# Kernel optimization log

Measured on AMD Instinct MI355X. Metric: run time of the kernel, lower is better.

## Reference

```python
import jax, jax.numpy as jnp
import numpy as np

B, D_IN, D, H, HD, M = 4096, 512, 128, 8, 16, 128
L = M + 1            # 1 query token + M memory slots
D_FF = 512
SCALE = 0.25         # 1/sqrt(HD)


def _ln(x, w, b, eps=1e-5):
    m = jnp.mean(x, axis=-1, keepdims=True)
    v = jnp.var(x, axis=-1, keepdims=True)
    return (x - m) * jax.lax.rsqrt(v + eps) * w + b


def setup_inputs() -> dict:
    ks = jax.random.split(jax.random.key(0), 26)
    n = lambda i, shape, s=1.0: jax.random.normal(ks[i], shape, jnp.float32) * s
    return {
        "x": n(0, (B, 1, D_IN)),
        "W_in": n(1, (D, D_IN), 0.05),
        "b_in": n(2, (D,), 0.02),
        "pos": n(3, (B, 1, D), 0.02),
        "mask": jnp.zeros((B, M), jnp.float32),  # additive attention bias for memory slots
        "mem": n(5, (B, M, D)),
        "ln1_w": jnp.ones((D,), jnp.float32), "ln1_b": jnp.zeros((D,), jnp.float32),
        "W_qkv": n(8, (3 * D, D), 0.09),
        "b_qkv": n(9, (3 * D,), 0.02),
        "W_out": n(10, (D, D), 0.09),
        "b_out": n(11, (D,), 0.02),
        "ln2_w": jnp.ones((D,), jnp.float32), "ln2_b": jnp.zeros((D,), jnp.float32),
        "ln3_w": jnp.ones((D,), jnp.float32), "ln3_b": jnp.zeros((D,), jnp.float32),
        "W_ff1": n(16, (D_FF, D), 0.09),
        "b_ff1": n(17, (D_FF,), 0.02),
        "ln4_w": jnp.ones((D_FF,), jnp.float32), "ln4_b": jnp.zeros((D_FF,), jnp.float32),
        "W_ff2": n(20, (D, D_FF), 0.04),
        "b_ff2": n(21, (D,), 0.02),
        "ln5_w": jnp.ones((D,), jnp.float32), "ln5_b": jnp.zeros((D,), jnp.float32),
        "W_head": n(24, (D_IN, D), 0.09),
        "b_head": n(25, (D_IN,), 0.02),
    }


def reference(x, W_in, b_in, pos, mask, mem, ln1_w, ln1_b, W_qkv, b_qkv,
              W_out, b_out, ln2_w, ln2_b, ln3_w, ln3_b, W_ff1, b_ff1,
              ln4_w, ln4_b, W_ff2, b_ff2, ln5_w, ln5_b, W_head, b_head):
    Bn = x.shape[0]
    # input projection + positional offset -> single query token per row  [B,1,D]
    q_in = (x.reshape(Bn, D_IN) @ W_in.T + b_in)[:, None, :] + pos
    # additive attention bias: 0 for the query slot, `mask` for memory slots  [B,L]
    bias = jnp.concatenate([jnp.zeros((Bn, 1), x.dtype), mask], axis=1)
    kv_in = jnp.concatenate([q_in, mem], axis=1)           # [B,L,D]
    kv_ln = _ln(kv_in, ln1_w, ln1_b)
    Wq, Wkv = W_qkv[:D], W_qkv[D:]
    bq, bkv = b_qkv[:D], b_qkv[D:]
    q = q_in[:, 0] @ Wq.T + bq                             # [B,D]  (Q uses UN-normalized q_in)
    kv = kv_ln @ Wkv.T + bkv                               # [B,L,2D]
    k, v = kv[..., :D], kv[..., D:]
    qh = q.reshape(Bn, H, HD)
    kh = k.reshape(Bn, L, H, HD)
    vh = v.reshape(Bn, L, H, HD)
    scores = jnp.einsum('bhd,blhd->bhl', qh * SCALE, kh) + bias[:, None, :]
    p = jax.nn.softmax(scores, axis=-1)                    # [B,H,L]
    o = jnp.einsum('bhl,blhd->bhd', p, vh).reshape(Bn, D)
    attn = _ln((o @ W_out.T + b_out)[:, None, :], ln2_w, ln2_b)
    h = attn + q_in                                        # residual  [B,1,D]
    f = _ln(h, ln3_w, ln3_b) @ W_ff1.T + b_ff1             # [B,1,D_FF]
    f = 0.5 * f * (1.0 + jax.lax.erf(f * 0.7071067811865476))  # exact GELU
    f = _ln(f, ln4_w, ln4_b) @ W_ff2.T + b_ff2             # [B,1,D]
    h2 = _ln(f + h, ln5_w, ln5_b)
    return h2 @ W_head.T + b_head                          # [B,1,D_IN]
```

## Files before the change

### kernel.cpp

```cpp
#include <hip/hip_runtime.h>

namespace {

constexpr int Dn   = 128;
constexpr int DIN  = 512;
constexpr int Hn   = 8;
constexpr int Mn   = 128;
constexpr int DFF  = 512;
constexpr int GC   = 8;
constexpr float ATT_SCALE = 0.25f;
constexpr float INV_SQRT2 = 0.70710678118654752440f;

typedef short  short8v  __attribute__((ext_vector_type(8)));
typedef float  float4v  __attribute__((ext_vector_type(4)));

__device__ __forceinline__ unsigned pk_bf16(float lo, float hi) {
    unsigned r;
    asm volatile("v_cvt_pk_bf16_f32 %0, %1, %2" : "=v"(r) : "v"(lo), "v"(hi));
    return r;
}
__device__ __forceinline__ float lo16(unsigned u) { return __uint_as_float(u << 16); }
__device__ __forceinline__ float hi16(unsigned u) { return __uint_as_float(u & 0xffff0000u); }

__device__ __forceinline__ float dot128(const float* __restrict__ wrow,
                                        const float* __restrict__ v)
{
    const float4* w4 = (const float4*)wrow;
    const float4* v4 = (const float4*)v;
    float acc = 0.f;
#pragma unroll
    for (int j = 0; j < 32; ++j) {
        float4 a = w4[j], b = v4[j];
        acc += a.x*b.x + a.y*b.y + a.z*b.z + a.w*b.w;
    }
    return acc;
}

template <int NCOL>
__device__ __forceinline__ void ln_row64(const float* __restrict__ src,
                                         float* __restrict__ dst,
                                         const float* __restrict__ gw,
                                         const float* __restrict__ gb,
                                         const float* __restrict__ resid,
                                         int sub)
{
    constexpr int E = NCOL / 64;
    float v0[E]; float sm = 0.f;
#pragma unroll
    for (int i = 0; i < E; ++i) { v0[i] = src[sub*E + i]; sm += v0[i]; }
#pragma unroll
    for (int m = 32; m >= 1; m >>= 1) sm += __shfl_xor(sm, m);
    float mean = sm * (1.f / (float)NCOL);
    float vs = 0.f;
#pragma unroll
    for (int i = 0; i < E; ++i) { float d0 = v0[i] - mean; vs += d0*d0; }
#pragma unroll
    for (int m = 32; m >= 1; m >>= 1) vs += __shfl_xor(vs, m);
    float rstd = rsqrtf(vs * (1.f / (float)NCOL) + 1e-5f);
#pragma unroll
    for (int i = 0; i < E; ++i) {
        int d = sub*E + i;
        float r = (v0[i] - mean) * rstd * gw[d] + gb[d];
        dst[d] = resid ? (r + resid[d]) : r;
    }
}

__global__ __launch_bounds__(256, 2)
void k_qin(const float* __restrict__ x, const float* __restrict__ W_in,
           const float* __restrict__ b_in, const float* __restrict__ pos,
           float* __restrict__ q_in)
{
    const int t  = threadIdx.x;
    const int b0 = blockIdx.x * 8;
    __shared__ __align__(16) float s_x[8 * DIN];
    {
        const float4* src = (const float4*)(x + (size_t)b0 * DIN);
        float4* dst = (float4*)s_x;
#pragma unroll
        for (int i = 0; i < 4; ++i) dst[t + 256*i] = src[t + 256*i];
    }
    __syncthreads();
    {
        int d = t & 127, gq = t >> 7;
        const float4* w4 = (const float4*)(W_in + (size_t)d * DIN);
        float acc[4] = {0,0,0,0};
        for (int j = 0; j < DIN/4; ++j) {
            float4 a = w4[j];
#pragma unroll
            for (int g = 0; g < 4; ++g) {
                float4 xv = ((const float4*)s_x)[(gq*4 + g)*(DIN/4) + j];
                acc[g] = fmaf(a.x, xv.x, acc[g]); acc[g] = fmaf(a.y, xv.y, acc[g]);
                acc[g] = fmaf(a.z, xv.z, acc[g]); acc[g] = fmaf(a.w, xv.w, acc[g]);
            }
        }
#pragma unroll
        for (int g = 0; g < 4; ++g) {
            int gb = b0 + gq*4 + g;
            q_in[(size_t)gb*Dn + d] = acc[g] + b_in[d] + pos[(size_t)gb*Dn + d];
        }
    }
}

__global__ __launch_bounds__(256, 2)
void k_attn(const float* __restrict__ q_in,
            const float* __restrict__ mask,
            const float* __restrict__ mem,
            const float* __restrict__ ln1_w, const float* __restrict__ ln1_b,
            const float* __restrict__ W_qkv, const float* __restrict__ b_qkv,
            float* __restrict__ o_ws)
{
    const int t    = threadIdx.x;
    const int lane = t & 63;
    const int wv   = t >> 6;
    const int b    = blockIdx.x;

    __shared__ __align__(16) unsigned short s16[Mn * Dn];
    __shared__ __align__(16) float s_X[1312];
    __shared__ __align__(16) float s_lnq[Dn];
    __shared__ __align__(16) float s_qi[Dn];
    __shared__ __align__(16) float s_q[Dn];
    __shared__ float s_s2c[Hn], s_s0[Hn], s_den[Hn], s_p0[Hn];

    unsigned short* s_At = (unsigned short*)s_X;
    float* s_sc = s_X;

    if (t < 32) ((float4*)s_qi)[t] = ((const float4*)(q_in + (size_t)b*Dn))[t];
    __syncthreads();

    {
        const float4* src = (const float4*)(mem + (size_t)b * Mn * Dn);
#pragma unroll
        for (int i = 0; i < 16; ++i) {
            int fid = t + 256*i;
            float4 v = src[fid];
            int r = fid >> 5, k = fid & 31;
            int c = k >> 1, half = k & 1;
            unsigned u0 = pk_bf16(v.x, v.y), u1 = pk_bf16(v.z, v.w);
            *(uint2*)&s16[r*128 + ((c ^ (r & 7)) << 3) + half*4] = make_uint2(u0, u1);
        }
    }
    if (t < 64) {
        ln_row64<Dn>(s_qi, s_lnq, ln1_w, ln1_b, nullptr, t);
    } else if (t >= 128) {
        int dd = t - 128;
        s_q[dd] = dot128(W_qkv + (size_t)dd*Dn, s_qi) + b_qkv[dd];
    }
    __syncthreads();

    {
        int h = t >> 5, js = t & 31;
        float aq[4] = {0,0,0,0};
        float ch = 0.f;
#pragma unroll
        for (int d0 = 0; d0 < 16; ++d0) {
            float qv = s_q[h*16 + d0];
            float4 w = ((const float4*)(W_qkv + (size_t)(Dn + h*16 + d0)*Dn))[js];
            aq[0] = fmaf(qv, w.x, aq[0]); aq[1] = fmaf(qv, w.y, aq[1]);
            aq[2] = fmaf(qv, w.z, aq[2]); aq[3] = fmaf(qv, w.w, aq[3]);
            ch = fmaf(qv, b_qkv[Dn + h*16 + d0], ch);
        }
        ch *= ATT_SCALE;
        float s1p = 0.f, s2p = 0.f, s0p = 0.f;
        float aqw[4];
#pragma unroll
        for (int c = 0; c < 4; ++c) {
            int j = js*4 + c;
            float a = ATT_SCALE * aq[c];
            aqw[c] = a * ln1_w[j];
            s1p += aqw[c];
            s2p = fmaf(a, ln1_b[j], s2p);
            s0p = fmaf(a, s_lnq[j], s0p);
        }
#pragma unroll
        for (int m = 16; m >= 1; m >>= 1) {
            s1p += __shfl_xor(s1p, m, 32);
            s2p += __shfl_xor(s2p, m, 32);
            s0p += __shfl_xor(s0p, m, 32);
        }
        float sub = s1p * (1.f/128.f);
        *(unsigned*)&s_At[h*136 + 4*js]     = pk_bf16(aqw[0]-sub, aqw[1]-sub);
        *(unsigned*)&s_At[h*136 + 4*js + 2] = pk_bf16(aqw[2]-sub, aqw[3]-sub);
        if (js == 0) { s_s2c[h] = s2p + ch; s_s0[h] = s0p + ch; }
        unsigned* X32 = (unsigned*)s_At;
        for (int idx = t; idx < 544; idx += 256) X32[8*68 + idx] = 0;
    }
    __syncthreads();

    float4v acc0 = {0.f,0.f,0.f,0.f}, acc1 = {0.f,0.f,0.f,0.f};
    float rstd_reg = 0.f;
    {
        const int al = lane & 15, ag = lane >> 4;
        const int r0 = (2*wv)*16 + al, r1 = (2*wv+1)*16 + al;
#pragma unroll
        for (int ks = 0; ks < 4; ++ks) {
            short8v af = *(const short8v*)&s_At[al*136 + ks*32 + ag*8];
            int c = ks*4 + ag;
            short8v b0 = *(const short8v*)&s16[r0*128 + ((c ^ (r0 & 7)) << 3)];
            short8v b1 = *(const short8v*)&s16[r1*128 + ((c ^ (r1 & 7)) << 3)];
            acc0 = __builtin_amdgcn_mfma_f32_16x16x32_bf16(af, b0, acc0, 0, 0, 0);
            acc1 = __builtin_amdgcn_mfma_f32_16x16x32_bf16(af, b1, acc1, 0, 0, 0);
        }
        int r = t >> 1, hf = t & 1;
        float sum = 0.f, ssq = 0.f;
#pragma unroll
        for (int kk = 0; kk < 8; ++kk) {
            int c = hf*8 + kk;
            uint4 tv = *(const uint4*)&s16[r*128 + ((c ^ (r & 7)) << 3)];
            float vv[8];
            vv[0] = lo16(tv.x); vv[1] = hi16(tv.x);
            vv[2] = lo16(tv.y); vv[3] = hi16(tv.y);
            vv[4] = lo16(tv.z); vv[5] = hi16(tv.z);
            vv[6] = lo16(tv.w); vv[7] = hi16(tv.w);
#pragma unroll
            for (int q = 0; q < 8; ++q) { sum += vv[q]; ssq = fmaf(vv[q], vv[q], ssq); }
        }
        sum += __shfl_xor(sum, 1);
        ssq += __shfl_xor(ssq, 1);
        float mean = sum * (1.f/128.f);
        float var  = fmaf(-mean, mean, ssq * (1.f/128.f));
        rstd_reg = rsqrtf(var + 1e-5f);
    }
    __syncthreads();

    {
        if (lane < 32) {
            int al = lane & 15, hb = (lane >> 4) * 4;
            int r0 = (2*wv)*16 + al, r1 = (2*wv+1)*16 + al;
#pragma unroll
            for (int reg = 0; reg < 4; ++reg) {
                s_sc[r0*10 + hb + reg] = acc0[reg];
                s_sc[r1*10 + hb + reg] = acc1[reg];
            }
        }
        if ((t & 1) == 0) s_sc[(t >> 1)*10 + 8] = rstd_reg;
    }
    __syncthreads();

    {
        int w = wv, l = lane;
        int h0 = 2*w, h1 = h0 + 1;
        int r0 = 2*l, r1 = r0 + 1;
        float2 da = *(const float2*)&s_sc[r0*10 + h0];
        float2 db = *(const float2*)&s_sc[r1*10 + h0];
        float rs0 = s_sc[r0*10 + 8], rs1 = s_sc[r1*10 + 8];
        float2 mk = *(const float2*)&mask[(size_t)b*Mn + r0];
        float sc00 = fmaf(rs0, da.x, s_s2c[h0]) + mk.x;
        float sc01 = fmaf(rs0, da.y, s_s2c[h1]) + mk.x;
        float sc10 = fmaf(rs1, db.x, s_s2c[h0]) + mk.y;
        float sc11 = fmaf(rs1, db.y, s_s2c[h1]) + mk.y;
        float mx0 = fmaxf(sc00, sc10), mx1 = fmaxf(sc01, sc11);
#pragma unroll
        for (int m = 1; m < 64; m <<= 1) {
            mx0 = fmaxf(mx0, __shfl_xor(mx0, m));
            mx1 = fmaxf(mx1, __shfl_xor(mx1, m));
        }
        mx0 = fmaxf(mx0, s_s0[h0]);
        mx1 = fmaxf(mx1, s_s0[h1]);
        float e00 = __expf(sc00 - mx0), e10 = __expf(sc10 - mx0);
        float e01 = __expf(sc01 - mx1), e11 = __expf(sc11 - mx1);
        float ds0 = e00 + e10, ds1 = e01 + e11;
#pragma unroll
        for (int m = 1; m < 64; m <<= 1) {
            ds0 += __shfl_xor(ds0, m);
            ds1 += __shfl_xor(ds1, m);
        }
        float p00 = __expf(s_s0[h0] - mx0), p01 = __expf(s_s0[h1] - mx1);
        *(float2*)&s_sc[r0*10 + h0] = make_float2(e00*rs0, e01*rs0);
        *(float2*)&s_sc[r1*10 + h0] = make_float2(e10*rs1, e11*rs1);
        if (l == 0) {
            s_den[h0] = ds0 + p00; s_p0[h0] = p00;
            s_den[h1] = ds1 + p01; s_p0[h1] = p01;
        }
    }
    __syncthreads();

    float cx0[8], cx1[8], cS0, cS1;
    {
        int w = wv, l = lane;
        int qtr = l >> 4, c = l & 15;
#pragma unroll
        for (int q = 0; q < 8; ++q) { cx0[q] = 0.f; cx1[q] = 0.f; }
#pragma unroll 4
        for (int rr = 0; rr < 32; ++rr) {
            int r = qtr*32 + rr;
            uint4 tv = *(const uint4*)&s16[r*128 + ((c ^ (r & 7)) << 3)];
            float2 qv = *(const float2*)&s_sc[r*10 + 2*w];
            float v0 = lo16(tv.x), v1 = hi16(tv.x);
            float v2 = lo16(tv.y), v3 = hi16(tv.y);
            float v4 = lo16(tv.z), v5 = hi16(tv.z);
            float v6 = lo16(tv.w), v7 = hi16(tv.w);
            cx0[0]=fmaf(qv.x,v0,cx0[0]); cx1[0]=fmaf(qv.y,v0,cx1[0]);
            cx0[1]=fmaf(qv.x,v1,cx0[1]); cx1[1]=fmaf(qv.y,v1,cx1[1]);
            cx0[2]=fmaf(qv.x,v2,cx0[2]); cx1[2]=fmaf(qv.y,v2,cx1[2]);
            cx0[3]=fmaf(qv.x,v3,cx0[3]); cx1[3]=fmaf(qv.y,v3,cx1[3]);
            cx0[4]=fmaf(qv.x,v4,cx0[4]); cx1[4]=fmaf(qv.y,v4,cx1[4]);
            cx0[5]=fmaf(qv.x,v5,cx0[5]); cx1[5]=fmaf(qv.y,v5,cx1[5]);
            cx0[6]=fmaf(qv.x,v6,cx0[6]); cx1[6]=fmaf(qv.y,v6,cx1[6]);
            cx0[7]=fmaf(qv.x,v7,cx0[7]); cx1[7]=fmaf(qv.y,v7,cx1[7]);
        }
#pragma unroll
        for (int q = 0; q < 8; ++q) {
            cx0[q] += __shfl_xor(cx0[q], 16);
            cx0[q] += __shfl_xor(cx0[q], 32);
            cx1[q] += __shfl_xor(cx1[q], 16);
            cx1[q] += __shfl_xor(cx1[q], 32);
        }
        float sA = ((cx0[0]+cx0[1])+(cx0[2]+cx0[3])) + ((cx0[4]+cx0[5])+(cx0[6]+cx0[7]));
        float sB = ((cx1[0]+cx1[1])+(cx1[2]+cx1[3])) + ((cx1[4]+cx1[5])+(cx1[6]+cx1[7]));
#pragma unroll
        for (int m = 1; m < 16; m <<= 1) {
            sA += __shfl_xor(sA, m);
            sB += __shfl_xor(sB, m);
        }
        cS0 = sA * (1.f/128.f);
        cS1 = sB * (1.f/128.f);
    }
    __syncthreads();

    if (lane < 16) {
        int c = lane;
        int h0 = 2*wv, h1 = h0 + 1;
        float den0 = s_den[h0], p0a = s_p0[h0], sP0 = den0 - p0a, inv0 = 1.f/den0;
        float den1 = s_den[h1], p0b = s_p0[h1], sP1 = den1 - p0b, inv1 = 1.f/den1;
#pragma unroll
        for (int q = 0; q < 2; ++q) {
            int j0 = c*8 + q*4;
            float4 lq = *(const float4*)&s_lnq[j0];
            float4 lw = *(const float4*)&ln1_w[j0];
            float4 lb = *(const float4*)&ln1_b[j0];
            float4 o0, o1;
            o0.x = (p0a*lq.x + lw.x*(cx0[q*4+0]-cS0) + lb.x*sP0) * inv0;
            o0.y = (p0a*lq.y + lw.y*(cx0[q*4+1]-cS0) + lb.y*sP0) * inv0;
            o0.z = (p0a*lq.z + lw.z*(cx0[q*4+2]-cS0) + lb.z*sP0) * inv0;
            o0.w = (p0a*lq.w + lw.w*(cx0[q*4+3]-cS0) + lb.w*sP0) * inv0;
            o1.x = (p0b*lq.x + lw.x*(cx1[q*4+0]-cS1) + lb.x*sP1) * inv1;
            o1.y = (p0b*lq.y + lw.y*(cx1[q*4+1]-cS1) + lb.y*sP1) * inv1;
            o1.z = (p0b*lq.z + lw.z*(cx1[q*4+2]-cS1) + lb.z*sP1) * inv1;
            o1.w = (p0b*lq.w + lw.w*(cx1[q*4+3]-cS1) + lb.w*sP1) * inv1;
            *(float4*)&s_X[h0*128 + j0] = o0;
            *(float4*)&s_X[h1*128 + j0] = o1;
        }
    }
    __syncthreads();

    {
        int d = t >> 1, half = t & 1;
        int h = d >> 4;
        const float4* w4 = (const float4*)(W_qkv + (size_t)(2*Dn + d)*Dn) + half*16;
        const float4* c4 = (const float4*)&s_X[h*128] + half*16;
        float acc = 0.f;
#pragma unroll
        for (int j = 0; j < 16; ++j) {
            float4 a = w4[j], v = c4[j];
            acc += a.x*v.x + a.y*v.y + a.z*v.z + a.w*v.w;
        }
        acc += __shfl_xor(acc, 1);
        if (half == 0)
            o_ws[(size_t)b*Dn + d] = acc + b_qkv[2*Dn + d];
    }
}

__global__ __launch_bounds__(256, 2)
void k_tail(const float* __restrict__ q_in, const float* __restrict__ o_ws,
            const float* __restrict__ W_out, const float* __restrict__ b_out,
            const float* __restrict__ ln2_w, const float* __restrict__ ln2_b,
            const float* __restrict__ ln3_w, const float* __restrict__ ln3_b,
            const float* __restrict__ W_ff1, const float* __restrict__ b_ff1,
            const float* __restrict__ ln4_w, const float* __restrict__ ln4_b,
            const float* __restrict__ W_ff2, const float* __restrict__ b_ff2,
            const float* __restrict__ ln5_w, const float* __restrict__ ln5_b,
            const float* __restrict__ W_head, const float* __restrict__ b_head,
            float* __restrict__ out)
{
    const int t    = threadIdx.x;
    const int lane = t & 63;
    const int wv   = t >> 6;
    const int b0   = blockIdx.x * GC;

    __shared__ __align__(16) float s_qi[GC][Dn];
    __shared__ __align__(16) float s_o [GC][Dn];
    __shared__ __align__(16) float s_t1[GC][Dn];
    __shared__ __align__(16) float s_h [GC][Dn];
    __shared__ __align__(16) float s_l3[GC][Dn];
    __shared__ __align__(16) float s_f1[GC * DFF];

    ((float4*)&s_qi[0][0])[t] = ((const float4*)(q_in + (size_t)b0*Dn))[t];
    ((float4*)&s_o [0][0])[t] = ((const float4*)(o_ws + (size_t)b0*Dn))[t];
    __syncthreads();

    {
        int d = t & 127, grp = t >> 7;
        const float4* w4 = (const float4*)(W_out + (size_t)d * Dn);
        float acc[4] = {0,0,0,0};
#pragma unroll 8
        for (int j = 0; j < 32; ++j) {
            float4 a = w4[j];
#pragma unroll
            for (int gg = 0; gg < 4; ++gg) {
                float4 v = *(const float4*)&s_o[grp*4 + gg][j*4];
                acc[gg] = fmaf(a.x,v.x,acc[gg]); acc[gg] = fmaf(a.y,v.y,acc[gg]);
                acc[gg] = fmaf(a.z,v.z,acc[gg]); acc[gg] = fmaf(a.w,v.w,acc[gg]);
            }
        }
#pragma unroll
        for (int gg = 0; gg < 4; ++gg) s_t1[grp*4 + gg][d] = acc[gg] + b_out[d];
    }
    __syncthreads();

    ln_row64<Dn>(&s_t1[wv][0], &s_h[wv][0], ln2_w, ln2_b, &s_qi[wv][0], lane);
    ln_row64<Dn>(&s_t1[wv+4][0], &s_h[wv+4][0], ln2_w, ln2_b, &s_qi[wv+4][0], lane);
    __syncthreads();
    ln_row64<Dn>(&s_h[wv][0], &s_l3[wv][0], ln3_w, ln3_b, nullptr, lane);
    ln_row64<Dn>(&s_h[wv+4][0], &s_l3[wv+4][0], ln3_w, ln3_b, nullptr, lane);
    __syncthreads();

    {
        int e0 = t, e1 = t + 256;
        const float4* wa = (const float4*)(W_ff1 + (size_t)e0 * Dn);
        const float4* wb = (const float4*)(W_ff1 + (size_t)e1 * Dn);
        float acc0[GC], acc1[GC];
#pragma unroll
        for (int g = 0; g < GC; ++g) { acc0[g] = 0.f; acc1[g] = 0.f; }
#pragma unroll 2
        for (int j = 0; j < 32; ++j) {
            float4 a = wa[j], bb = wb[j];
#pragma unroll
            for (int g = 0; g < GC; ++g) {
                float4 v = *(const float4*)&s_l3[g][j*4];
                acc0[g] = fmaf(a.x,v.x,acc0[g]);  acc0[g] = fmaf(a.y,v.y,acc0[g]);
                acc0[g] = fmaf(a.z,v.z,acc0[g]);  acc0[g] = fmaf(a.w,v.w,acc0[g]);
                acc1[g] = fmaf(bb.x,v.x,acc1[g]); acc1[g] = fmaf(bb.y,v.y,acc1[g]);
                acc1[g] = fmaf(bb.z,v.z,acc1[g]); acc1[g] = fmaf(bb.w,v.w,acc1[g]);
            }
        }
#pragma unroll
        for (int g = 0; g < GC; ++g) {
            float v0 = acc0[g] + b_ff1[e0];
            float v1 = acc1[g] + b_ff1[e1];
            s_f1[g*DFF + e0] = 0.5f * v0 * (1.f + erff(v0 * INV_SQRT2));
            s_f1[g*DFF + e1] = 0.5f * v1 * (1.f + erff(v1 * INV_SQRT2));
        }
    }
    __syncthreads();

    ln_row64<DFF>(&s_f1[wv*DFF], &s_f1[wv*DFF], ln4_w, ln4_b, nullptr, lane);
    ln_row64<DFF>(&s_f1[(wv+4)*DFF], &s_f1[(wv+4)*DFF], ln4_w, ln4_b, nullptr, lane);
    __syncthreads();

    {
        int d = t & 127, grp = t >> 7;
        const float4* w4 = (const float4*)(W_ff2 + (size_t)d * DFF);
        float acc[4] = {0,0,0,0};
#pragma unroll 4
        for (int j = 0; j < DFF/4; ++j) {
            float4 a = w4[j];
#pragma unroll
            for (int gg = 0; gg < 4; ++gg) {
                float4 v = ((const float4*)&s_f1[(grp*4 + gg)*DFF])[j];
                acc[gg] = fmaf(a.x,v.x,acc[gg]); acc[gg] = fmaf(a.y,v.y,acc[gg]);
                acc[gg] = fmaf(a.z,v.z,acc[gg]); acc[gg] = fmaf(a.w,v.w,acc[gg]);
            }
        }
#pragma unroll
        for (int gg = 0; gg < 4; ++gg)
            s_t1[grp*4 + gg][d] = acc[gg] + b_ff2[d] + s_h[grp*4 + gg][d];
    }
    __syncthreads();

    ln_row64<Dn>(&s_t1[wv][0], &s_o[wv][0], ln5_w, ln5_b, nullptr, lane);
    ln_row64<Dn>(&s_t1[wv+4][0], &s_o[wv+4][0], ln5_w, ln5_b, nullptr, lane);
    __syncthreads();

    {
        int e0 = t, e1 = t + 256;
        const float4* wa = (const float4*)(W_head + (size_t)e0 * Dn);
        const float4* wb = (const float4*)(W_head + (size_t)e1 * Dn);
        float acc0[GC], acc1[GC];
#pragma unroll
        for (int g = 0; g < GC; ++g) { acc0[g] = 0.f; acc1[g] = 0.f; }
#pragma unroll 2
        for (int j = 0; j < 32; ++j) {
            float4 a = wa[j], bb = wb[j];
#pragma unroll
            for (int g = 0; g < GC; ++g) {
                float4 v = *(const float4*)&s_o[g][j*4];
                acc0[g] = fmaf(a.x,v.x,acc0[g]);  acc0[g] = fmaf(a.y,v.y,acc0[g]);
                acc0[g] = fmaf(a.z,v.z,acc0[g]);  acc0[g] = fmaf(a.w,v.w,acc0[g]);
                acc1[g] = fmaf(bb.x,v.x,acc1[g]); acc1[g] = fmaf(bb.y,v.y,acc1[g]);
                acc1[g] = fmaf(bb.z,v.z,acc1[g]); acc1[g] = fmaf(bb.w,v.w,acc1[g]);
            }
        }
#pragma unroll
        for (int g = 0; g < GC; ++g) {
            out[(size_t)(b0+g)*DIN + e0] = acc0[g] + b_head[e0];
            out[(size_t)(b0+g)*DIN + e1] = acc1[g] + b_head[e1];
        }
    }
}

}

extern "C" void kernel_launch(void* const* d_in, const int* in_sizes, int n_in,
                              void* d_out, int out_size, void* d_ws, size_t ws_size,
                              hipStream_t stream)
{
    const float* x      = (const float*)d_in[0];
    const float* W_in   = (const float*)d_in[1];
    const float* b_in   = (const float*)d_in[2];
    const float* pos    = (const float*)d_in[3];
    const float* mask   = (const float*)d_in[4];
    const float* mem    = (const float*)d_in[5];
    const float* ln1_w  = (const float*)d_in[6];
    const float* ln1_b  = (const float*)d_in[7];
    const float* W_qkv  = (const float*)d_in[8];
    const float* b_qkv  = (const float*)d_in[9];
    const float* W_out  = (const float*)d_in[10];
    const float* b_out  = (const float*)d_in[11];
    const float* ln2_w  = (const float*)d_in[12];
    const float* ln2_b  = (const float*)d_in[13];
    const float* ln3_w  = (const float*)d_in[14];
    const float* ln3_b  = (const float*)d_in[15];
    const float* W_ff1  = (const float*)d_in[16];
    const float* b_ff1  = (const float*)d_in[17];
    const float* ln4_w  = (const float*)d_in[18];
    const float* ln4_b  = (const float*)d_in[19];
    const float* W_ff2  = (const float*)d_in[20];
    const float* b_ff2  = (const float*)d_in[21];
    const float* ln5_w  = (const float*)d_in[22];
    const float* ln5_b  = (const float*)d_in[23];
    const float* W_head = (const float*)d_in[24];
    const float* b_head = (const float*)d_in[25];

    const int B = in_sizes[0] / DIN;
    float* ws_qin = (float*)d_ws;
    float* ws_o   = (float*)d_ws + (size_t)B * Dn;

    k_qin<<<dim3(B / 8), dim3(256), 0, stream>>>(x, W_in, b_in, pos, ws_qin);
    k_attn<<<dim3(B), dim3(256), 0, stream>>>(ws_qin, mask, mem,
                                              ln1_w, ln1_b, W_qkv, b_qkv, ws_o);
    k_tail<<<dim3(B / GC), dim3(256), 0, stream>>>(ws_qin, ws_o,
        W_out, b_out, ln2_w, ln2_b, ln3_w, ln3_b,
        W_ff1, b_ff1, ln4_w, ln4_b, W_ff2, b_ff2,
        ln5_w, ln5_b, W_head, b_head, (float*)d_out);
}
```

Before: 254.3 us.

## Double k_attn block to 512 threads, one wave per attention head

Widens the attention kernel from 256 to 512 threads per block (8 waves) and remaps every phase so that each wave owns one head instead of two. Each thread now loads half as many memory rows, runs one MFMA chain instead of two, and handles a single head in softmax and PV. The goal is more memory-level parallelism and latency hiding per block while holding about 33KB of LDS. The cost is more block-wide syncs across more waves, and occupancy may be limited by registers or LDS under launch_bounds(512,2).

```diff
diff --git a/kernel.cpp b/kernel.cpp
--- a/kernel.cpp
+++ b/kernel.cpp
@@ -101,7 +101,7 @@
     }
 }
 
-__global__ __launch_bounds__(256, 2)
+__global__ __launch_bounds__(512, 2)
 void k_attn(const float* __restrict__ q_in,
             const float* __restrict__ mask,
             const float* __restrict__ mem,
@@ -130,8 +130,8 @@
     {
         const float4* src = (const float4*)(mem + (size_t)b * Mn * Dn);
 #pragma unroll
-        for (int i = 0; i < 16; ++i) {
-            int fid = t + 256*i;
+        for (int i = 0; i < 8; ++i) {
+            int fid = t + 512*i;
             float4 v = src[fid];
             int r = fid >> 5, k = fid & 31;
             int c = k >> 1, half = k & 1;
@@ -141,70 +141,63 @@
     }
     if (t < 64) {
         ln_row64<Dn>(s_qi, s_lnq, ln1_w, ln1_b, nullptr, t);
-    } else if (t >= 128) {
+    } else if (t >= 128 && t < 256) {
         int dd = t - 128;
         s_q[dd] = dot128(W_qkv + (size_t)dd*Dn, s_qi) + b_qkv[dd];
     }
     __syncthreads();
 
     {
-        int h = t >> 5, js = t & 31;
-        float aq[4] = {0,0,0,0};
-        float ch = 0.f;
+        int h = wv, l = lane;
+        float aq0 = 0.f, aq1 = 0.f, ch = 0.f;
 #pragma unroll
         for (int d0 = 0; d0 < 16; ++d0) {
             float qv = s_q[h*16 + d0];
-            float4 w = ((const float4*)(W_qkv + (size_t)(Dn + h*16 + d0)*Dn))[js];
-            aq[0] = fmaf(qv, w.x, aq[0]); aq[1] = fmaf(qv, w.y, aq[1]);
-            aq[2] = fmaf(qv, w.z, aq[2]); aq[3] = fmaf(qv, w.w, aq[3]);
-            ch = fmaf(qv, b_qkv[Dn + h*16 + d0], ch);
+            float2 w2 = *(const float2*)&W_qkv[(size_t)(Dn + h*16 + d0)*Dn + 2*l];
+            aq0 = fmaf(qv, w2.x, aq0);
+            aq1 = fmaf(qv, w2.y, aq1);
+            ch  = fmaf(qv, b_qkv[Dn + h*16 + d0], ch);
         }
         ch *= ATT_SCALE;
-        float s1p = 0.f, s2p = 0.f, s0p = 0.f;
-        float aqw[4];
-#pragma unroll
-        for (int c = 0; c < 4; ++c) {
-            int j = js*4 + c;
-            float a = ATT_SCALE * aq[c];
-            aqw[c] = a * ln1_w[j];
-            s1p += aqw[c];
-            s2p = fmaf(a, ln1_b[j], s2p);
-            s0p = fmaf(a, s_lnq[j], s0p);
-        }
-#pragma unroll
-        for (int m = 16; m >= 1; m >>= 1) {
-            s1p += __shfl_xor(s1p, m, 32);
-            s2p += __shfl_xor(s2p, m, 32);
-            s0p += __shfl_xor(s0p, m, 32);
+        float a0 = ATT_SCALE * aq0, a1 = ATT_SCALE * aq1;
+        float2 lw = *(const float2*)&ln1_w[2*l];
+        float2 lb = *(const float2*)&ln1_b[2*l];
+        float2 lq = *(const float2*)&s_lnq[2*l];
+        float aqw0 = a0 * lw.x, aqw1 = a1 * lw.y;
+        float s1p = aqw0 + aqw1;
+        float s2p = a0*lb.x + a1*lb.y;
+        float s0p = a0*lq.x + a1*lq.y;
+#pragma unroll
+        for (int m = 32; m >= 1; m >>= 1) {
+            s1p += __shfl_xor(s1p, m);
+            s2p += __shfl_xor(s2p, m);
+            s0p += __shfl_xor(s0p, m);
         }
         float sub = s1p * (1.f/128.f);
-        *(unsigned*)&s_At[h*136 + 4*js]     = pk_bf16(aqw[0]-sub, aqw[1]-sub);
-        *(unsigned*)&s_At[h*136 + 4*js + 2] = pk_bf16(aqw[2]-sub, aqw[3]-sub);
-        if (js == 0) { s_s2c[h] = s2p + ch; s_s0[h] = s0p + ch; }
+        *(unsigned*)&s_At[h*136 + 2*l] = pk_bf16(aqw0 - sub, aqw1 - sub);
+        if (l == 0) { s_s2c[h] = s2p + ch; s_s0[h] = s0p + ch; }
         unsigned* X32 = (unsigned*)s_At;
-        for (int idx = t; idx < 544; idx += 256) X32[8*68 + idx] = 0;
-    }
-    __syncthreads();
-
-    float4v acc0 = {0.f,0.f,0.f,0.f}, acc1 = {0.f,0.f,0.f,0.f};
+        for (int idx = t; idx < 544; idx += 512) X32[8*68 + idx] = 0;
+    }
+    __syncthreads();
+
+    float4v acc0 = {0.f,0.f,0.f,0.f};
     float rstd_reg = 0.f;
     {
         const int al = lane & 15, ag = lane >> 4;
-        const int r0 = (2*wv)*16 + al, r1 = (2*wv+1)*16 + al;
+        const int r0 = wv*16 + al;
 #pragma unroll
         for (int ks = 0; ks < 4; ++ks) {
             short8v af = *(const short8v*)&s_At[al*136 + ks*32 + ag*8];
             int c = ks*4 + ag;
             short8v b0 = *(const short8v*)&s16[r0*128 + ((c ^ (r0 & 7)) << 3)];
-            short8v b1 = *(const short8v*)&s16[r1*128 + ((c ^ (r1 & 7)) << 3)];
             acc0 = __builtin_amdgcn_mfma_f32_16x16x32_bf16(af, b0, acc0, 0, 0, 0);
-            acc1 = __builtin_amdgcn_mfma_f32_16x16x32_bf16(af, b1, acc1, 0, 0, 0);
-        }
-        int r = t >> 1, hf = t & 1;
+        }
+        int r = t >> 2, hf = t & 3;
         float sum = 0.f, ssq = 0.f;
 #pragma unroll
-        for (int kk = 0; kk < 8; ++kk) {
-            int c = hf*8 + kk;
+        for (int kk = 0; kk < 4; ++kk) {
+            int c = hf*4 + kk;
             uint4 tv = *(const uint4*)&s16[r*128 + ((c ^ (r & 7)) << 3)];
             float vv[8];
             vv[0] = lo16(tv.x); vv[1] = hi16(tv.x);
@@ -214,8 +207,8 @@
 #pragma unroll
             for (int q = 0; q < 8; ++q) { sum += vv[q]; ssq = fmaf(vv[q], vv[q], ssq); }
         }
-        sum += __shfl_xor(sum, 1);
-        ssq += __shfl_xor(ssq, 1);
+        sum += __shfl_xor(sum, 1); sum += __shfl_xor(sum, 2);
+        ssq += __shfl_xor(ssq, 1); ssq += __shfl_xor(ssq, 2);
         float mean = sum * (1.f/128.f);
         float var  = fmaf(-mean, mean, ssq * (1.f/128.f));
         rstd_reg = rsqrtf(var + 1e-5f);
@@ -225,137 +218,103 @@
     {
         if (lane < 32) {
             int al = lane & 15, hb = (lane >> 4) * 4;
-            int r0 = (2*wv)*16 + al, r1 = (2*wv+1)*16 + al;
-#pragma unroll
-            for (int reg = 0; reg < 4; ++reg) {
+            int r0 = wv*16 + al;
+#pragma unroll
+            for (int reg = 0; reg < 4; ++reg)
                 s_sc[r0*10 + hb + reg] = acc0[reg];
-                s_sc[r1*10 + hb + reg] = acc1[reg];
-            }
-        }
-        if ((t & 1) == 0) s_sc[(t >> 1)*10 + 8] = rstd_reg;
+        }
+        if ((t & 3) == 0) s_sc[(t >> 2)*10 + 8] = rstd_reg;
     }
     __syncthreads();
 
     {
         int w = wv, l = lane;
-        int h0 = 2*w, h1 = h0 + 1;
         int r0 = 2*l, r1 = r0 + 1;
-        float2 da = *(const float2*)&s_sc[r0*10 + h0];
-        float2 db = *(const float2*)&s_sc[r1*10 + h0];
-        float rs0 = s_sc[r0*10 + 8], rs1 = s_sc[r1*10 + 8];
+        float d0 = s_sc[r0*10 + w], rs0 = s_sc[r0*10 + 8];
+        float d1 = s_sc[r1*10 + w], rs1 = s_sc[r1*10 + 8];
         float2 mk = *(const float2*)&mask[(size_t)b*Mn + r0];
-        float sc00 = fmaf(rs0, da.x, s_s2c[h0]) + mk.x;
-        float sc01 = fmaf(rs0, da.y, s_s2c[h1]) + mk.x;
-        float sc10 = fmaf(rs1, db.x, s_s2c[h0]) + mk.y;
-        float sc11 = fmaf(rs1, db.y, s_s2c[h1]) + mk.y;
-        float mx0 = fmaxf(sc00, sc10), mx1 = fmaxf(sc01, sc11);
-#pragma unroll
-        for (int m = 1; m < 64; m <<= 1) {
-            mx0 = fmaxf(mx0, __shfl_xor(mx0, m));
-            mx1 = fmaxf(mx1, __shfl_xor(mx1, m));
-        }
-        mx0 = fmaxf(mx0, s_s0[h0]);
-        mx1 = fmaxf(mx1, s_s0[h1]);
-        float e00 = __expf(sc00 - mx0), e10 = __expf(sc10 - mx0);
-        float e01 = __expf(sc01 - mx1), e11 = __expf(sc11 - mx1);
-        float ds0 = e00 + e10, ds1 = e01 + e11;
-#pragma unroll
-        for (int m = 1; m < 64; m <<= 1) {
-            ds0 += __shfl_xor(ds0, m);
-            ds1 += __shfl_xor(ds1, m);
-        }
-        float p00 = __expf(s_s0[h0] - mx0), p01 = __expf(s_s0[h1] - mx1);
-        *(float2*)&s_sc[r0*10 + h0] = make_float2(e00*rs0, e01*rs0);
-        *(float2*)&s_sc[r1*10 + h0] = make_float2(e10*rs1, e11*rs1);
-        if (l == 0) {
-            s_den[h0] = ds0 + p00; s_p0[h0] = p00;
-            s_den[h1] = ds1 + p01; s_p0[h1] = p01;
-        }
-    }
-    __syncthreads();
-
-    float cx0[8], cx1[8], cS0, cS1;
+        float sc0 = fmaf(rs0, d0, s_s2c[w]) + mk.x;
+        float sc1 = fmaf(rs1, d1, s_s2c[w]) + mk.y;
+        float mx = fmaxf(sc0, sc1);
+#pragma unroll
+        for (int m = 1; m < 64; m <<= 1) mx = fmaxf(mx, __shfl_xor(mx, m));
+        mx = fmaxf(mx, s_s0[w]);
+        float e0 = __expf(sc0 - mx), e1 = __expf(sc1 - mx);
+        float ds = e0 + e1;
+#pragma unroll
+        for (int m = 1; m < 64; m <<= 1) ds += __shfl_xor(ds, m);
+        float p0 = __expf(s_s0[w] - mx);
+        s_sc[r0*10 + w] = e0 * rs0;
+        s_sc[r1*10 + w] = e1 * rs1;
+        if (l == 0) { s_den[w] = ds + p0; s_p0[w] = p0; }
+    }
+    __syncthreads();
+
+    float cx[8], cS;
     {
         int w = wv, l = lane;
         int qtr = l >> 4, c = l & 15;
 #pragma unroll
-        for (int q = 0; q < 8; ++q) { cx0[q] = 0.f; cx1[q] = 0.f; }
+        for (int q = 0; q < 8; ++q) cx[q] = 0.f;
 #pragma unroll 4
         for (int rr = 0; rr < 32; ++rr) {
             int r = qtr*32 + rr;
             uint4 tv = *(const uint4*)&s16[r*128 + ((c ^ (r & 7)) << 3)];
-            float2 qv = *(const float2*)&s_sc[r*10 + 2*w];
-            float v0 = lo16(tv.x), v1 = hi16(tv.x);
-            float v2 = lo16(tv.y), v3 = hi16(tv.y);
-            float v4 = lo16(tv.z), v5 = hi16(tv.z);
-            float v6 = lo16(tv.w), v7 = hi16(tv.w);
-            cx0[0]=fmaf(qv.x,v0,cx0[0]); cx1[0]=fmaf(qv.y,v0,cx1[0]);
-            cx0[1]=fmaf(qv.x,v1,cx0[1]); cx1[1]=fmaf(qv.y,v1,cx1[1]);
-            cx0[2]=fmaf(qv.x,v2,cx0[2]); cx1[2]=fmaf(qv.y,v2,cx1[2]);
-            cx0[3]=fmaf(qv.x,v3,cx0[3]); cx1[3]=fmaf(qv.y,v3,cx1[3]);
-            cx0[4]=fmaf(qv.x,v4,cx0[4]); cx1[4]=fmaf(qv.y,v4,cx1[4]);
-            cx0[5]=fmaf(qv.x,v5,cx0[5]); cx1[5]=fmaf(qv.y,v5,cx1[5]);
-            cx0[6]=fmaf(qv.x,v6,cx0[6]); cx1[6]=fmaf(qv.y,v6,cx1[6]);
-            cx0[7]=fmaf(qv.x,v7,cx0[7]); cx1[7]=fmaf(qv.y,v7,cx1[7]);
+            float qv = s_sc[r*10 + w];
+            cx[0] = fmaf(qv, lo16(tv.x), cx[0]);
+            cx[1] = fmaf(qv, hi16(tv.x), cx[1]);
+            cx[2] = fmaf(qv, lo16(tv.y), cx[2]);
+            cx[3] = fmaf(qv, hi16(tv.y), cx[3]);
+            cx[4] = fmaf(qv, lo16(tv.z), cx[4]);
+            cx[5] = fmaf(qv, hi16(tv.z), cx[5]);
+            cx[6] = fmaf(qv, lo16(tv.w), cx[6]);
+            cx[7] = fmaf(qv, hi16(tv.w), cx[7]);
         }
 #pragma unroll
         for (int q = 0; q < 8; ++q) {
-            cx0[q] += __shfl_xor(cx0[q], 16);
-            cx0[q] += __shfl_xor(cx0[q], 32);
-            cx1[q] += __shfl_xor(cx1[q], 16);
-            cx1[q] += __shfl_xor(cx1[q], 32);
-        }
-        float sA = ((cx0[0]+cx0[1])+(cx0[2]+cx0[3])) + ((cx0[4]+cx0[5])+(cx0[6]+cx0[7]));
-        float sB = ((cx1[0]+cx1[1])+(cx1[2]+cx1[3])) + ((cx1[4]+cx1[5])+(cx1[6]+cx1[7]));
-#pragma unroll
-        for (int m = 1; m < 16; m <<= 1) {
-            sA += __shfl_xor(sA, m);
-            sB += __shfl_xor(sB, m);
-        }
-        cS0 = sA * (1.f/128.f);
-        cS1 = sB * (1.f/128.f);
+            cx[q] += __shfl_xor(cx[q], 16);
+            cx[q] += __shfl_xor(cx[q], 32);
+        }
+        float sA = ((cx[0]+cx[1])+(cx[2]+cx[3])) + ((cx[4]+cx[5])+(cx[6]+cx[7]));
+#pragma unroll
+        for (int m = 1; m < 16; m <<= 1) sA += __shfl_xor(sA, m);
+        cS = sA * (1.f/128.f);
     }
     __syncthreads();
 
     if (lane < 16) {
-        int c = lane;
-        int h0 = 2*wv, h1 = h0 + 1;
-        float den0 = s_den[h0], p0a = s_p0[h0], sP0 = den0 - p0a, inv0 = 1.f/den0;
-        float den1 = s_den[h1], p0b = s_p0[h1], sP1 = den1 - p0b, inv1 = 1.f/den1;
+        int c = lane, w = wv;
+        float den = s_den[w], p0a = s_p0[w], sP = den - p0a, inv = 1.f/den;
 #pragma unroll
         for (int q = 0; q < 2; ++q) {
             int j0 = c*8 + q*4;
             float4 lq = *(const float4*)&s_lnq[j0];
             float4 lw = *(const float4*)&ln1_w[j0];
             float4 lb = *(const float4*)&ln1_b[j0];
-            float4 o0, o1;
-            o0.x = (p0a*lq.x + lw.x*(cx0[q*4+0]-cS0) + lb.x*sP0) * inv0;
-            o0.y = (p0a*lq.y + lw.y*(cx0[q*4+1]-cS0) + lb.y*sP0) * inv0;
-            o0.z = (p0a*lq.z + lw.z*(cx0[q*4+2]-cS0) + lb.z*sP0) * inv0;
-            o0.w = (p0a*lq.w + lw.w*(cx0[q*4+3]-cS0) + lb.w*sP0) * inv0;
-            o1.x = (p0b*lq.x + lw.x*(cx1[q*4+0]-cS1) + lb.x*sP1) * inv1;
-            o1.y = (p0b*lq.y + lw.y*(cx1[q*4+1]-cS1) + lb.y*sP1) * inv1;
-            o1.z = (p0b*lq.z + lw.z*(cx1[q*4+2]-cS1) + lb.z*sP1) * inv1;
-            o1.w = (p0b*lq.w + lw.w*(cx1[q*4+3]-cS1) + lb.w*sP1) * inv1;
-            *(float4*)&s_X[h0*128 + j0] = o0;
-            *(float4*)&s_X[h1*128 + j0] = o1;
-        }
-    }
-    __syncthreads();
-
-    {
-        int d = t >> 1, half = t & 1;
+            float4 o0;
+            o0.x = (p0a*lq.x + lw.x*(cx[q*4+0]-cS) + lb.x*sP) * inv;
+            o0.y = (p0a*lq.y + lw.y*(cx[q*4+1]-cS) + lb.y*sP) * inv;
+            o0.z = (p0a*lq.z + lw.z*(cx[q*4+2]-cS) + lb.z*sP) * inv;
+            o0.w = (p0a*lq.w + lw.w*(cx[q*4+3]-cS) + lb.w*sP) * inv;
+            *(float4*)&s_X[w*128 + j0] = o0;
+        }
+    }
+    __syncthreads();
+
+    {
+        int d = t >> 2, q4 = t & 3;
         int h = d >> 4;
-        const float4* w4 = (const float4*)(W_qkv + (size_t)(2*Dn + d)*Dn) + half*16;
-        const float4* c4 = (const float4*)&s_X[h*128] + half*16;
+        const float4* w4 = (const float4*)(W_qkv + (size_t)(2*Dn + d)*Dn) + q4*8;
+        const float4* c4 = (const float4*)&s_X[h*128] + q4*8;
         float acc = 0.f;
 #pragma unroll
-        for (int j = 0; j < 16; ++j) {
+        for (int j = 0; j < 8; ++j) {
             float4 a = w4[j], v = c4[j];
             acc += a.x*v.x + a.y*v.y + a.z*v.z + a.w*v.w;
         }
         acc += __shfl_xor(acc, 1);
-        if (half == 0)
+        acc += __shfl_xor(acc, 2);
+        if (q4 == 0)
             o_ws[(size_t)b*Dn + d] = acc + b_qkv[2*Dn + d];
     }
 }
@@ -536,7 +495,7 @@
     float* ws_o   = (float*)d_ws + (size_t)B * Dn;
 
     k_qin<<<dim3(B / 8), dim3(256), 0, stream>>>(x, W_in, b_in, pos, ws_qin);
-    k_attn<<<dim3(B), dim3(256), 0, stream>>>(ws_qin, mask, mem,
+    k_attn<<<dim3(B), dim3(512), 0, stream>>>(ws_qin, mask, mem,
                                               ln1_w, ln1_b, W_qkv, b_qkv, ws_o);
     k_tail<<<dim3(B / GC), dim3(256), 0, stream>>>(ws_qin, ws_o,
         W_out, b_out, ln2_w, ln2_b, ln3_w, ln3_b,
```

Measured after the change: 243.3 us, median of 2. -4.3%, faster.
